# Performance work log

Hardware: AMD Instinct MI355X
Metric: run time of the kernel (lower is better)

## Reference

```python
import jax, jax.numpy as jnp
import numpy as np

H_SIZE = 64  # height_pad == width_pad == 64 (power of 2, no padding needed)


def _hadamard(n):
    H = np.array([[1.0]], dtype=np.float32)
    while H.shape[0] < n:
        H = np.block([[H, H], [H, -H]])
    return jnp.asarray(H)


def setup_inputs() -> dict:
    key = jax.random.key(0)
    k1, k2, k3, k4 = jax.random.split(key, 4)
    B, C_in, C_out, P = 32, 256, 256, 2
    x = jax.random.normal(k1, (B, C_in, H_SIZE, H_SIZE), dtype=jnp.float32)
    v = jax.random.uniform(k2, (P, H_SIZE, H_SIZE), dtype=jnp.float32)
    W = jax.random.normal(k3, (P, C_out, C_in), dtype=jnp.float32) * (1.0 / np.sqrt(C_in))
    T = jax.random.uniform(k4, (P, H_SIZE, H_SIZE), dtype=jnp.float32) * 0.1
    return {"x": x, "v": v, "W": W, "T": T}


def reference(x, v, W, T):
    n = H_SIZE
    H = _hadamard(n)  # symmetric, H @ H = n * I
    # 2D WHT: apply along width then height
    f1 = jnp.einsum('bchw,wk->bchk', x, H)
    f2 = jnp.einsum('bchw,hk->bckw', f1, H)
    # per-pod: scale, 1x1 conv, soft-threshold
    f3 = v[:, None, None, :, :] * f2[None]                 # (p,b,c,h,w)
    f4 = jnp.einsum('poc,pbchw->pbohw', W, f3)             # 1x1 conv, no bias
    f5 = jnp.sign(f4) * jnp.maximum(jnp.abs(f4) - T[:, None, None, :, :], 0.0)
    f6 = f5.sum(axis=0)                                     # sum over pods
    # inverse 2D WHT (H^{-1} = H / n)
    f7 = jnp.einsum('bchw,wk->bchk', f6, H) / n
    f8 = jnp.einsum('bchw,hk->bckw', f7, H) / n
    return f8 + x  # residual
```

## Files before the change

### kernel.cpp

```cpp
#include <hip/hip_runtime.h>
#include <stdint.h>


typedef __attribute__((ext_vector_type(4))) float f32x4_t;
typedef __attribute__((ext_vector_type(8))) __bf16 bf16x8_t;
typedef __attribute__((ext_vector_type(8))) unsigned short u16x8_t;
typedef __attribute__((ext_vector_type(4))) unsigned short u16x4_t;

__device__ __forceinline__ float bf2f(unsigned short u) {
  union { unsigned int i; float f; } x; x.i = ((unsigned int)u) << 16; return x.f;
}
__device__ __forceinline__ unsigned short f2bf(float f) {
  union { float f; unsigned int i; } x; x.f = f;
  unsigned int i = x.i;
  return (unsigned short)((i + 0x7FFFu + ((i >> 16) & 1u)) >> 16);
}
__device__ __forceinline__ unsigned short f2bf_t(float f) {
  union { float f; unsigned int i; } x; x.f = f;
  return (unsigned short)(x.i >> 16);
}
__device__ __forceinline__ size_t Faddr(size_t f) {
  return ((f >> 12) << 13) + 4096 + (f & 4095);
}

__global__ __launch_bounds__(512) void k_fwd(const float* __restrict__ x,
                                             unsigned short* __restrict__ obuf) {
  __shared__ unsigned short smem[36864];
  int tid = threadIdx.x;
  int lane = tid & 63, wave = tid >> 6;
  int quad = lane >> 4, l15 = lane & 15;
  int cg = blockIdx.x, b = blockIdx.y;
  size_t img = (size_t)b * 256 + cg * 8 + wave;
  unsigned short* T1t = smem + wave * 4608;

  const float* xim = x + img * 4096;
#pragma unroll
  for (int l = 0; l < 16; l++) {
    int e = (l * 64 + lane) * 4;
    f32x4_t sv = *(const f32x4_t*)(xim + e);
    u16x4_t u;
#pragma unroll
    for (int j = 0; j < 4; j++) u[j] = f2bf_t(sv[j]);
    int row = e >> 6, col = e & 63;
    *(u16x4_t*)&T1t[row * 72 + col] = u;
  }

  bf16x8_t hf[2][4];
#pragma unroll
  for (int kc = 0; kc < 2; kc++)
#pragma unroll
    for (int t = 0; t < 4; t++) {
      bf16x8_t h;
#pragma unroll
      for (int j = 0; j < 8; j++) {
        int k = kc * 32 + quad * 8 + j, n = t * 16 + l15;
        h[j] = (__builtin_popcount(k & n) & 1) ? (__bf16)-1.0f : (__bf16)1.0f;
      }
      hf[kc][t] = h;
    }

  bf16x8_t xa[4][2];
#pragma unroll
  for (int mt = 0; mt < 4; mt++)
#pragma unroll
    for (int kc = 0; kc < 2; kc++)
      xa[mt][kc] = *(const bf16x8_t*)&T1t[(mt * 16 + l15) * 72 + kc * 32 + quad * 8];

#pragma unroll
  for (int nt = 0; nt < 4; nt++) {
    f32x4_t a1c[4];
#pragma unroll
    for (int mt = 0; mt < 4; mt++) a1c[mt] = (f32x4_t){0.f, 0.f, 0.f, 0.f};
#pragma unroll
    for (int kc = 0; kc < 2; kc++)
#pragma unroll
      for (int mt = 0; mt < 4; mt++)
        a1c[mt] = __builtin_amdgcn_mfma_f32_16x16x32_bf16(xa[mt][kc], hf[kc][nt], a1c[mt], 0, 0, 0);
#pragma unroll
    for (int mt = 0; mt < 4; mt++) {
      u16x4_t t4;
#pragma unroll
      for (int r = 0; r < 4; r++) t4[r] = f2bf_t(a1c[mt][r]);
      *(u16x4_t*)&T1t[(nt * 16 + l15) * 72 + mt * 16 + quad * 4] = t4;
    }
  }

  f32x4_t acc[4][4];
#pragma unroll
  for (int mt = 0; mt < 4; mt++)
#pragma unroll
    for (int nt = 0; nt < 4; nt++) acc[mt][nt] = (f32x4_t){0.f, 0.f, 0.f, 0.f};
#pragma unroll
  for (int kc = 0; kc < 2; kc++)
#pragma unroll
    for (int nt = 0; nt < 4; nt++) {
      bf16x8_t bfr = *(bf16x8_t*)&T1t[(nt * 16 + l15) * 72 + kc * 32 + quad * 8];
#pragma unroll
      for (int mt = 0; mt < 4; mt++)
        acc[mt][nt] = __builtin_amdgcn_mfma_f32_16x16x32_bf16(hf[kc][mt], bfr, acc[mt][nt], 0, 0, 0);
    }

  __syncthreads();
#pragma unroll
  for (int mt = 0; mt < 4; mt++)
#pragma unroll
    for (int nt = 0; nt < 4; nt++)
#pragma unroll
      for (int r = 0; r < 4; r++) {
        int pos = (mt * 16 + quad * 4 + r) * 64 + nt * 16 + l15;
        smem[pos * 8 + wave] = f2bf(acc[mt][nt][r]);
      }
  __syncthreads();
  size_t fbase = ((size_t)b * 32 + cg) * 4096;
#pragma unroll
  for (int i = 0; i < 8; i++) {
    int pos = i * 512 + tid;
    u16x8_t vch = *(u16x8_t*)&smem[pos * 8];
    *(u16x8_t*)(obuf + Faddr((fbase + pos) * 8)) = vch;
  }
}

__global__ __launch_bounds__(256) void k_gemm(const float* __restrict__ Wf,
                                              const float* __restrict__ vv,
                                              const float* __restrict__ TT,
                                              unsigned short* __restrict__ obuf) {
  __shared__ unsigned short smem2[32768];
  int tid = threadIdx.x;
  int lane = tid & 63, wave = tid >> 6;
  int quad = lane >> 4, l15 = lane & 15;
  int wm = wave & 1, wn = wave >> 1;
  int n0 = blockIdx.x * 128;
  int m0 = blockIdx.y * 128;
  int b  = blockIdx.z;

  f32x4_t acc[4][4];
#pragma unroll
  for (int mt = 0; mt < 4; mt++)
#pragma unroll
    for (int nt = 0; nt < 4; nt++) acc[mt][nt] = (f32x4_t){0.f, 0.f, 0.f, 0.f};

  auto issueB = [&](int ks, int buf) {
    unsigned short* Bl = smem2 + 16384 + buf * 8192;
#pragma unroll
    for (int i = 0; i < 4; i++) {
      int idx = i * 256 + tid;
      int r = idx & 127, cch = idx >> 7;
      size_t f = (((size_t)b * 32 + ks * 8 + cch) * 4096 + n0 + r) * 8;
      const unsigned short* src = obuf + Faddr(f);
      __builtin_amdgcn_global_load_lds(
          (const __attribute__((address_space(1))) void*)src,
          (__attribute__((address_space(3))) void*)(Bl + idx * 8), 16, 0, 0);
    }
  };
  auto fetchA = [&](int ks, f32x4_t (&ar)[4][2]) {
    int k0 = ks * 64;
#pragma unroll
    for (int i = 0; i < 4; i++) {
      int idx = i * 256 + tid;
      int r = idx >> 3, cch = idx & 7;
      int gch = cch ^ (r & 7);
      int m = m0 + r;
      const float* wp = Wf + ((m & 1) << 16) + ((m >> 1) << 8) + k0 + gch * 8;
      ar[i][0] = *(const f32x4_t*)wp;
      ar[i][1] = *(const f32x4_t*)(wp + 4);
    }
  };
  auto writeA = [&](int buf, f32x4_t (&ar)[4][2]) {
    unsigned short* Al = smem2 + buf * 8192;
#pragma unroll
    for (int i = 0; i < 4; i++) {
      int idx = i * 256 + tid;
      u16x8_t u;
#pragma unroll
      for (int j = 0; j < 4; j++) { u[j] = f2bf_t(ar[i][0][j]); u[4 + j] = f2bf_t(ar[i][1][j]); }
      *(u16x8_t*)&Al[idx * 8] = u;
    }
  };

  f32x4_t areg[4][2];
  issueB(0, 0);
  fetchA(0, areg);
  writeA(0, areg);
  __syncthreads();

  for (int ks = 0; ks < 4; ++ks) {
    int p = ks & 1;
    if (ks < 3) {
      issueB(ks + 1, p ^ 1);
      fetchA(ks + 1, areg);
    }
    unsigned short* Al = smem2 + p * 8192;
    unsigned short* Bl = smem2 + 16384 + p * 8192;
#pragma unroll
    for (int kk = 0; kk < 2; ++kk) {
      bf16x8_t af[4], bfr[4];
#pragma unroll
      for (int mt = 0; mt < 4; mt++) {
        int row = wm * 64 + mt * 16 + l15;
        int s = (kk * 4 + quad) ^ (row & 7);
        af[mt] = *(const bf16x8_t*)&Al[row * 64 + s * 8];
      }
      int ch = kk * 4 + quad;
#pragma unroll
      for (int nt = 0; nt < 4; nt++)
        bfr[nt] = *(const bf16x8_t*)&Bl[ch * 1024 + (wn * 64 + nt * 16 + l15) * 8];
#pragma unroll
      for (int mt = 0; mt < 4; mt++)
#pragma unroll
        for (int nt = 0; nt < 4; nt++)
          acc[mt][nt] = __builtin_amdgcn_mfma_f32_16x16x32_bf16(af[mt], bfr[nt], acc[mt][nt], 0, 0, 0);
    }
    if (ks < 3) writeA(p ^ 1, areg);
    __syncthreads();
  }

#pragma unroll
  for (int nt = 0; nt < 4; nt++) {
    int posl = wn * 64 + nt * 16 + l15;
    int pos = n0 + posl;
    float v0 = vv[pos], v1 = vv[4096 + pos];
    float t0 = TT[pos], t1 = TT[4096 + pos];
#pragma unroll
    for (int mt = 0; mt < 4; mt++)
#pragma unroll
      for (int rp = 0; rp < 2; rp++) {
        int ol = wm * 32 + mt * 8 + quad * 2 + rp;
        float z0 = acc[mt][nt][rp * 2 + 0] * v0;
        float z1 = acc[mt][nt][rp * 2 + 1] * v1;
        float s0 = copysignf(fmaxf(fabsf(z0) - t0, 0.f), z0);
        float s1 = copysignf(fmaxf(fabsf(z1) - t1, 0.f), z1);
        smem2[ol * 136 + posl] = f2bf(s0 + s1);
      }
  }
  __syncthreads();
  int o0 = m0 >> 1;
#pragma unroll
  for (int i = 0; i < 4; i++) {
    int ci = i * 256 + tid;
    int row = ci >> 4, cc = ci & 15;
    u16x8_t vch = *(u16x8_t*)&smem2[row * 136 + cc * 8];
    size_t img = (size_t)b * 256 + o0 + row;
    *(u16x8_t*)(obuf + img * 8192 + n0 + cc * 8) = vch;
  }
}

__global__ __launch_bounds__(256) void k_inv(const float* __restrict__ x,
                                             unsigned short* __restrict__ obuf) {
  __shared__ unsigned short smem[18432];
  int tid = threadIdx.x;
  int lane = tid & 63, wave = tid >> 6;
  int quad = lane >> 4, l15 = lane & 15;
  size_t img = (size_t)blockIdx.x * 4 + wave;
  unsigned short* T1t = smem + wave * 4608;

#pragma unroll
  for (int l = 0; l < 8; l++) {
    int e = (l * 64 + lane) * 8;
    u16x8_t sv = *(const u16x8_t*)(obuf + img * 8192 + e);
    int row = e >> 6, col = e & 63;
    *(u16x8_t*)&T1t[row * 72 + col] = sv;
  }

  bf16x8_t hf[2][4];
#pragma unroll
  for (int kc = 0; kc < 2; kc++)
#pragma unroll
    for (int t = 0; t < 4; t++) {
      bf16x8_t h;
#pragma unroll
      for (int j = 0; j < 8; j++) {
        int k = kc * 32 + quad * 8 + j, n = t * 16 + l15;
        h[j] = (__builtin_popcount(k & n) & 1) ? (__bf16)-1.0f : (__bf16)1.0f;
      }
      hf[kc][t] = h;
    }

  bf16x8_t fa[4][2];
#pragma unroll
  for (int mt = 0; mt < 4; mt++)
#pragma unroll
    for (int kc = 0; kc < 2; kc++)
      fa[mt][kc] = *(const bf16x8_t*)&T1t[(mt * 16 + l15) * 72 + kc * 32 + quad * 8];

#pragma unroll
  for (int nt = 0; nt < 4; nt++) {
    f32x4_t a1c[4];
#pragma unroll
    for (int mt = 0; mt < 4; mt++) a1c[mt] = (f32x4_t){0.f, 0.f, 0.f, 0.f};
#pragma unroll
    for (int kc = 0; kc < 2; kc++)
#pragma unroll
      for (int mt = 0; mt < 4; mt++)
        a1c[mt] = __builtin_amdgcn_mfma_f32_16x16x32_bf16(fa[mt][kc], hf[kc][nt], a1c[mt], 0, 0, 0);
#pragma unroll
    for (int mt = 0; mt < 4; mt++) {
      u16x4_t t4;
#pragma unroll
      for (int r = 0; r < 4; r++) t4[r] = f2bf_t(a1c[mt][r]);
      *(u16x4_t*)&T1t[(nt * 16 + l15) * 72 + mt * 16 + quad * 4] = t4;
    }
  }

  f32x4_t acc[4][4];
#pragma unroll
  for (int mt = 0; mt < 4; mt++)
#pragma unroll
    for (int nt = 0; nt < 4; nt++) acc[mt][nt] = (f32x4_t){0.f, 0.f, 0.f, 0.f};
#pragma unroll
  for (int kc = 0; kc < 2; kc++)
#pragma unroll
    for (int nt = 0; nt < 4; nt++) {
      bf16x8_t bfr = *(bf16x8_t*)&T1t[(nt * 16 + l15) * 72 + kc * 32 + quad * 8];
#pragma unroll
      for (int mt = 0; mt < 4; mt++)
        acc[mt][nt] = __builtin_amdgcn_mfma_f32_16x16x32_bf16(hf[kc][mt], bfr, acc[mt][nt], 0, 0, 0);
    }

  const float sc = 1.0f / 4096.0f;
#pragma unroll
  for (int mt = 0; mt < 4; mt++)
#pragma unroll
    for (int nt = 0; nt < 4; nt++)
#pragma unroll
      for (int r = 0; r < 4; r++)
        T1t[(mt * 16 + quad * 4 + r) * 72 + nt * 16 + l15] = f2bf(acc[mt][nt][r] * sc);

  float* outf = (float*)obuf;
  const float* xim = x + img * 4096;
#pragma unroll
  for (int l = 0; l < 8; l++) {
    int e = (l * 64 + lane) * 8;
    int row = e >> 6, col = e & 63;
    u16x8_t tv = *(u16x8_t*)&T1t[row * 72 + col];
    f32x4_t x0 = *(const f32x4_t*)(xim + e);
    f32x4_t x1 = *(const f32x4_t*)(xim + e + 4);
    f32x4_t o0, o1;
#pragma unroll
    for (int j = 0; j < 4; j++) { o0[j] = bf2f(tv[j]) + x0[j]; o1[j] = bf2f(tv[4 + j]) + x1[j]; }
    *(f32x4_t*)(outf + img * 4096 + e) = o0;
    *(f32x4_t*)(outf + img * 4096 + e + 4) = o1;
  }
}

extern "C" void kernel_launch(void* const* d_in, const int* in_sizes, int n_in,
                              void* d_out, int out_size, void* d_ws, size_t ws_size,
                              hipStream_t stream) {
  const float* x = (const float*)d_in[0];
  const float* v = (const float*)d_in[1];
  const float* W = (const float*)d_in[2];
  const float* T = (const float*)d_in[3];
  unsigned short* obuf = (unsigned short*)d_out;
  (void)d_ws; (void)ws_size; (void)in_sizes; (void)n_in; (void)out_size;

  k_fwd<<<dim3(32, 32), 512, 0, stream>>>(x, obuf);
  k_gemm<<<dim3(32, 4, 32), 256, 0, stream>>>(W, v, T, obuf);
  k_inv<<<2048, 256, 0, stream>>>(x, obuf);
}
```

Before: 333.5 us.

## Swizzle forward-transform LDS staging and single-buffer the A tile in GEMM

In the forward WHT kernel, the per-wave bf16 scatter into shared memory now uses an XOR swizzle on the channel slot to spread bank accesses. The readback un-permutes the 32-bit pairs with a per-iteration index so the global layout stays the same. In the GEMM kernel, the A (weight) tile goes from double-buffered to single-buffered LDS, cutting shared memory from 64KB to 48KB, likely to raise occupancy. The price is an extra __syncthreads per k-step before and after writing A.

```diff
diff --git a/kernel.cpp b/kernel.cpp
--- a/kernel.cpp
+++ b/kernel.cpp
@@ -6,6 +6,7 @@
 typedef __attribute__((ext_vector_type(8))) __bf16 bf16x8_t;
 typedef __attribute__((ext_vector_type(8))) unsigned short u16x8_t;
 typedef __attribute__((ext_vector_type(4))) unsigned short u16x4_t;
+typedef __attribute__((ext_vector_type(4))) unsigned int u32x4_t;
 
 __device__ __forceinline__ float bf2f(unsigned short u) {
   union { unsigned int i; float f; } x; x.i = ((unsigned int)u) << 16; return x.f;
@@ -108,15 +109,31 @@
 #pragma unroll
       for (int r = 0; r < 4; r++) {
         int pos = (mt * 16 + quad * 4 + r) * 64 + nt * 16 + l15;
-        smem[pos * 8 + wave] = f2bf(acc[mt][nt][r]);
+        smem[pos * 8 + (wave ^ (quad << 1))] = f2bf(acc[mt][nt][r]);
       }
   __syncthreads();
   size_t fbase = ((size_t)b * 32 + cg) * 4096;
-#pragma unroll
-  for (int i = 0; i < 8; i++) {
-    int pos = i * 512 + tid;
-    u16x8_t vch = *(u16x8_t*)&smem[pos * 8];
-    *(u16x8_t*)(obuf + Faddr((fbase + pos) * 8)) = vch;
+  int hb = wave >> 2;
+  if (hb) {
+#pragma unroll
+    for (int i = 0; i < 8; i++) {
+      int pos = i * 512 + tid;
+      u32x4_t c = *(u32x4_t*)&smem[pos * 8];
+      const int q = (2 * i + 1) & 3;
+      u32x4_t o;
+      o[0] = c[0 ^ q]; o[1] = c[1 ^ q]; o[2] = c[2 ^ q]; o[3] = c[3 ^ q];
+      *(u32x4_t*)(obuf + Faddr((fbase + pos) * 8)) = o;
+    }
+  } else {
+#pragma unroll
+    for (int i = 0; i < 8; i++) {
+      int pos = i * 512 + tid;
+      u32x4_t c = *(u32x4_t*)&smem[pos * 8];
+      const int q = (2 * i) & 3;
+      u32x4_t o;
+      o[0] = c[0 ^ q]; o[1] = c[1 ^ q]; o[2] = c[2 ^ q]; o[3] = c[3 ^ q];
+      *(u32x4_t*)(obuf + Faddr((fbase + pos) * 8)) = o;
+    }
   }
 }
 
@@ -124,7 +141,8 @@
                                               const float* __restrict__ vv,
                                               const float* __restrict__ TT,
                                               unsigned short* __restrict__ obuf) {
-  __shared__ unsigned short smem2[32768];
+  __shared__ unsigned short smem2[24576];
+  unsigned short* Alds = smem2;
   int tid = threadIdx.x;
   int lane = tid & 63, wave = tid >> 6;
   int quad = lane >> 4, l15 = lane & 15;
@@ -140,7 +158,7 @@
     for (int nt = 0; nt < 4; nt++) acc[mt][nt] = (f32x4_t){0.f, 0.f, 0.f, 0.f};
 
   auto issueB = [&](int ks, int buf) {
-    unsigned short* Bl = smem2 + 16384 + buf * 8192;
+    unsigned short* Bl = smem2 + 8192 + buf * 8192;
 #pragma unroll
     for (int i = 0; i < 4; i++) {
       int idx = i * 256 + tid;
@@ -165,22 +183,21 @@
       ar[i][1] = *(const f32x4_t*)(wp + 4);
     }
   };
-  auto writeA = [&](int buf, f32x4_t (&ar)[4][2]) {
-    unsigned short* Al = smem2 + buf * 8192;
+  auto writeA = [&](f32x4_t (&ar)[4][2]) {
 #pragma unroll
     for (int i = 0; i < 4; i++) {
       int idx = i * 256 + tid;
       u16x8_t u;
 #pragma unroll
       for (int j = 0; j < 4; j++) { u[j] = f2bf_t(ar[i][0][j]); u[4 + j] = f2bf_t(ar[i][1][j]); }
-      *(u16x8_t*)&Al[idx * 8] = u;
+      *(u16x8_t*)&Alds[idx * 8] = u;
     }
   };
 
   f32x4_t areg[4][2];
   issueB(0, 0);
   fetchA(0, areg);
-  writeA(0, areg);
+  writeA(areg);
   __syncthreads();
 
   for (int ks = 0; ks < 4; ++ks) {
@@ -189,8 +206,7 @@
       issueB(ks + 1, p ^ 1);
       fetchA(ks + 1, areg);
     }
-    unsigned short* Al = smem2 + p * 8192;
-    unsigned short* Bl = smem2 + 16384 + p * 8192;
+    unsigned short* Bl = smem2 + 8192 + p * 8192;
 #pragma unroll
     for (int kk = 0; kk < 2; ++kk) {
       bf16x8_t af[4], bfr[4];
@@ -198,7 +214,7 @@
       for (int mt = 0; mt < 4; mt++) {
         int row = wm * 64 + mt * 16 + l15;
         int s = (kk * 4 + quad) ^ (row & 7);
-        af[mt] = *(const bf16x8_t*)&Al[row * 64 + s * 8];
+        af[mt] = *(const bf16x8_t*)&Alds[row * 64 + s * 8];
       }
       int ch = kk * 4 + quad;
 #pragma unroll
@@ -210,8 +226,11 @@
         for (int nt = 0; nt < 4; nt++)
           acc[mt][nt] = __builtin_amdgcn_mfma_f32_16x16x32_bf16(af[mt], bfr[nt], acc[mt][nt], 0, 0, 0);
     }
-    if (ks < 3) writeA(p ^ 1, areg);
     __syncthreads();
+    if (ks < 3) {
+      writeA(areg);
+      __syncthreads();
+    }
   }
 
 #pragma unroll
```

Result: no change. 334.3 us (+0.2%).
